# Kernel optimization log

Hardware: AMD Instinct MI355X
Metric: run time of the kernel (lower is better)

The kernel has to match this reference:

```python
import jax, jax.numpy as jnp
import numpy as np
from jax import lax

SIGMA = 2.0
RADIUS = 8  # int(truncate(4.0)*sigma + 0.5) per scipy gaussian_filter

_x = np.arange(-RADIUS, RADIUS + 1, dtype=np.float32)
_gw = np.exp(-0.5 * (_x / SIGMA) ** 2)
GAUSS_W = jnp.asarray(_gw / _gw.sum(), dtype=jnp.float32)  # 17 taps, sums to 1
DERIV_W = jnp.asarray([-1.0, 0.0, 1.0], dtype=jnp.float32)   # scipy correlate1d [-1,0,1]
SMOOTH_W = jnp.asarray([1.0, 2.0, 1.0], dtype=jnp.float32)

DN = ('NCHW', 'OIHW', 'NCHW')

def _corr_h(img, w, pad_mode):
    # 1D cross-correlation along H axis of [B,1,H,W]
    r = w.shape[0] // 2
    p = jnp.pad(img, ((0, 0), (0, 0), (r, r), (0, 0)), mode=pad_mode)
    k = w.reshape(1, 1, -1, 1)
    return lax.conv_general_dilated(p, k, (1, 1), 'VALID', dimension_numbers=DN)

def _corr_w(img, w, pad_mode):
    # 1D cross-correlation along W axis of [B,1,H,W]
    r = w.shape[0] // 2
    p = jnp.pad(img, ((0, 0), (0, 0), (0, 0), (r, r)), mode=pad_mode)
    k = w.reshape(1, 1, 1, -1)
    return lax.conv_general_dilated(p, k, (1, 1), 'VALID', dimension_numbers=DN)

def setup_inputs() -> dict:
    key = jax.random.key(0)
    x = jax.random.normal(key, (32, 3, 512, 512), dtype=jnp.float32)
    return {"x": x}

def reference(x) -> jnp.ndarray:
    # channel mean -> [B,1,H,W]
    g = jnp.mean(x, axis=1, keepdims=True)
    # gaussian blur, scipy mode='reflect' == numpy/jnp 'symmetric' padding
    blur = _corr_w(_corr_h(g, GAUSS_W, 'symmetric'), GAUSS_W, 'symmetric')
    # scipy sobel, mode='constant' (zero pad): deriv along given axis, [1,2,1] smooth along other
    sx = _corr_w(_corr_h(blur, DERIV_W, 'constant'), SMOOTH_W, 'constant')  # axis=0 (H)
    sy = _corr_h(_corr_w(blur, DERIV_W, 'constant'), SMOOTH_W, 'constant')  # axis=1 (W)
    return jnp.hypot(sx, sy)  # [B,1,H,W]
```

## Files before the change

kernel.cpp:

```cpp
#include <hip/hip_runtime.h>
#include <math.h>

#define IMG   512
#define TILE  64
#define HALO  9
#define BROWS 66
#define BSTR  83
#define CSTR  67

__device__ __forceinline__ int reflect_idx(int i) {
    if (i < 0) i = -i - 1;
    if (i >= IMG) i = 2 * IMG - 1 - i;
    return i;
}

__global__ __launch_bounds__(256) void sobel_fused(
    const float* __restrict__ x, float* __restrict__ out)
{
    __shared__ float sB[BROWS * BSTR];
    __shared__ float sC[BROWS * CSTR];

    const int t  = threadIdx.x;
    const int w0 = blockIdx.x * TILE;
    const int h0 = blockIdx.y * TILE;
    const int b  = blockIdx.z;

    const float ge[9] = {1.0f, 0.882496903f, 0.606530660f, 0.324652467f,
                         0.135335283f, 0.0439369336f, 0.0111089965f,
                         0.00218749112f, 0.000335462628f};
    float gw[17];
    {
        float s = 0.f;
        #pragma unroll
        for (int i = 0; i < 17; ++i) { gw[i] = ge[(i < 8) ? (8 - i) : (i - 8)]; s += gw[i]; }
        float inv = 1.0f / s;
        #pragma unroll
        for (int i = 0; i < 17; ++i) gw[i] *= inv;
    }

    const float* xb = x + (size_t)b * 3 * IMG * IMG;
    const float third = 1.0f / 3.0f;

    if (t < 246) {
        int c   = t % 82;
        int seg = t / 82;
        int r0  = seg * 22;
        int gc  = reflect_idx(w0 - HALO + c);
        const float* p0 = xb + gc;
        float v[38];
        #pragma unroll
        for (int i = 0; i < 38; ++i) {
            int gr = reflect_idx(h0 - HALO + r0 + i);
            const float* p = p0 + (size_t)gr * IMG;
            v[i] = (p[0] + p[IMG * IMG] + p[2 * IMG * IMG]) * third;
        }
        #pragma unroll
        for (int j = 0; j < 22; ++j) {
            float a = 0.f;
            #pragma unroll
            for (int k = 0; k < 17; ++k) a += gw[k] * v[j + k];
            sB[(r0 + j) * BSTR + c] = a;
        }
    }
    __syncthreads();

    if (t < 198) {
        int r   = t % 66;
        int seg = t / 66;
        int c0  = seg * 22;
        float v[38];
        #pragma unroll
        for (int i = 0; i < 38; ++i) v[i] = sB[r * BSTR + c0 + i];
        int gr = h0 - 1 + r;
        bool rin = (gr >= 0) & (gr < IMG);
        #pragma unroll
        for (int j = 0; j < 22; ++j) {
            float a = 0.f;
            #pragma unroll
            for (int k = 0; k < 17; ++k) a += gw[k] * v[j + k];
            int gc = w0 - 1 + c0 + j;
            bool in = rin & (gc >= 0) & (gc < IMG);
            sC[r * CSTR + c0 + j] = in ? a : 0.f;
        }
    }
    __syncthreads();

    {
        int c  = t & 63;
        int rq = t >> 6;
        #pragma unroll
        for (int it = 0; it < 4; ++it) {
            int r0 = (rq + it * 4) * 4;
            const float* bp = sC + r0 * CSTR + c;
            float m[6][3];
            #pragma unroll
            for (int rr = 0; rr < 6; ++rr) {
                #pragma unroll
                for (int cc = 0; cc < 3; ++cc)
                    m[rr][cc] = bp[rr * CSTR + cc];
            }
            #pragma unroll
            for (int dr = 0; dr < 4; ++dr) {
                float tl = m[dr][0],   tm = m[dr][1],   tr = m[dr][2];
                float ml = m[dr+1][0],                  mr = m[dr+1][2];
                float bl = m[dr+2][0], bm = m[dr+2][1], br2 = m[dr+2][2];
                float sx = (bl - tl) + 2.f * (bm - tm) + (br2 - tr);
                float sy = (tr - tl) + 2.f * (mr - ml) + (br2 - bl);
                out[((size_t)b * IMG + (h0 + r0 + dr)) * IMG + (w0 + c)]
                    = sqrtf(sx * sx + sy * sy);
            }
        }
    }
}

extern "C" void kernel_launch(void* const* d_in, const int* in_sizes, int n_in,
                              void* d_out, int out_size, void* d_ws, size_t ws_size,
                              hipStream_t stream) {
    const float* x = (const float*)d_in[0];
    float* out = (float*)d_out;
    dim3 grid(IMG / TILE, IMG / TILE, 32);
    dim3 block(256);
    hipLaunchKernelGGL(sobel_fused, grid, block, 0, stream, x, out);
}
```

Before: 167.6 us.

## Blur along W first with float4 row loads, then H from shared memory

Swaps the separable Gaussian pass order so the first pass runs along rows. Each thread loads a contiguous row segment with float4 vector loads over the three channels, which replaces the scalar strided column loads of the old H-first pass. A scalar reflect fallback handles tiles at the image edges. The shared-memory layout changes to match, and launch bounds now request 4 blocks per SM, which may force register spills given the 40-element per-thread arrays.

```diff
diff --git a/kernel.cpp b/kernel.cpp
--- a/kernel.cpp
+++ b/kernel.cpp
@@ -5,8 +5,8 @@
 #define TILE  64
 #define HALO  9
 #define BROWS 66
-#define BSTR  83
-#define CSTR  67
+#define MROWS 82
+#define SSTR  67
 
 __device__ __forceinline__ int reflect_idx(int i) {
     if (i < 0) i = -i - 1;
@@ -14,11 +14,11 @@
     return i;
 }
 
-__global__ __launch_bounds__(256) void sobel_fused(
+__global__ __launch_bounds__(256, 4) void sobel_fused(
     const float* __restrict__ x, float* __restrict__ out)
 {
-    __shared__ float sB[BROWS * BSTR];
-    __shared__ float sC[BROWS * CSTR];
+    __shared__ float sB[MROWS * SSTR];
+    __shared__ float sC[BROWS * SSTR];
 
     const int t  = threadIdx.x;
     const int w0 = blockIdx.x * TILE;
@@ -42,45 +42,68 @@
     const float third = 1.0f / 3.0f;
 
     if (t < 246) {
-        int c   = t % 82;
+        int r   = t % 82;
         int seg = t / 82;
+        int c0  = seg * 24;
+        int gr  = reflect_idx(h0 - HALO + r);
+        const float* rowp = xb + (size_t)gr * IMG;
+        int startc = w0 + c0 - HALO;
+        int abase  = startc - 3;
+        float v[40];
+        if (abase >= 0 && abase + 44 <= IMG) {
+            const float* pa = rowp + abase;
+            #pragma unroll
+            for (int q = 0; q < 11; ++q) {
+                float4 a = *(const float4*)(pa + 4 * q);
+                float4 bb = *(const float4*)(pa + IMG * IMG + 4 * q);
+                float4 cc = *(const float4*)(pa + 2 * IMG * IMG + 4 * q);
+                float m0 = (a.x + bb.x + cc.x) * third;
+                float m1 = (a.y + bb.y + cc.y) * third;
+                float m2 = (a.z + bb.z + cc.z) * third;
+                float m3 = (a.w + bb.w + cc.w) * third;
+                int i0 = 4 * q - 3;
+                if (i0 >= 0)      v[i0]     = m0;
+                if (i0 + 1 >= 0)  v[i0 + 1] = m1;
+                if (i0 + 2 >= 0)  v[i0 + 2] = m2;
+                if (i0 + 3 < 40)  v[i0 + 3] = m3;
+            }
+        } else {
+            #pragma unroll
+            for (int i = 0; i < 40; ++i) {
+                int gc = reflect_idx(startc + i);
+                const float* p = rowp + gc;
+                v[i] = (p[0] + p[IMG * IMG] + p[2 * IMG * IMG]) * third;
+            }
+        }
+        #pragma unroll
+        for (int j = 0; j < 24; ++j) {
+            if (c0 + j < BROWS) {
+                float a = 0.f;
+                #pragma unroll
+                for (int k = 0; k < 17; ++k) a += gw[k] * v[j + k];
+                sB[r * SSTR + c0 + j] = a;
+            }
+        }
+    }
+    __syncthreads();
+
+    if (t < 198) {
+        int c   = t % 66;
+        int seg = t / 66;
         int r0  = seg * 22;
-        int gc  = reflect_idx(w0 - HALO + c);
-        const float* p0 = xb + gc;
         float v[38];
         #pragma unroll
-        for (int i = 0; i < 38; ++i) {
-            int gr = reflect_idx(h0 - HALO + r0 + i);
-            const float* p = p0 + (size_t)gr * IMG;
-            v[i] = (p[0] + p[IMG * IMG] + p[2 * IMG * IMG]) * third;
-        }
+        for (int i = 0; i < 38; ++i) v[i] = sB[(r0 + i) * SSTR + c];
+        int gcol = w0 - 1 + c;
+        bool cin = (gcol >= 0) & (gcol < IMG);
         #pragma unroll
         for (int j = 0; j < 22; ++j) {
             float a = 0.f;
             #pragma unroll
             for (int k = 0; k < 17; ++k) a += gw[k] * v[j + k];
-            sB[(r0 + j) * BSTR + c] = a;
-        }
-    }
-    __syncthreads();
-
-    if (t < 198) {
-        int r   = t % 66;
-        int seg = t / 66;
-        int c0  = seg * 22;
-        float v[38];
-        #pragma unroll
-        for (int i = 0; i < 38; ++i) v[i] = sB[r * BSTR + c0 + i];
-        int gr = h0 - 1 + r;
-        bool rin = (gr >= 0) & (gr < IMG);
-        #pragma unroll
-        for (int j = 0; j < 22; ++j) {
-            float a = 0.f;
-            #pragma unroll
-            for (int k = 0; k < 17; ++k) a += gw[k] * v[j + k];
-            int gc = w0 - 1 + c0 + j;
-            bool in = rin & (gc >= 0) & (gc < IMG);
-            sC[r * CSTR + c0 + j] = in ? a : 0.f;
+            int grow = h0 - 1 + r0 + j;
+            bool in = cin & (grow >= 0) & (grow < IMG);
+            sC[(r0 + j) * SSTR + c] = in ? a : 0.f;
         }
     }
     __syncthreads();
@@ -91,13 +114,13 @@
         #pragma unroll
         for (int it = 0; it < 4; ++it) {
             int r0 = (rq + it * 4) * 4;
-            const float* bp = sC + r0 * CSTR + c;
+            const float* bp = sC + r0 * SSTR + c;
             float m[6][3];
             #pragma unroll
             for (int rr = 0; rr < 6; ++rr) {
                 #pragma unroll
                 for (int cc = 0; cc < 3; ++cc)
-                    m[rr][cc] = bp[rr * CSTR + cc];
+                    m[rr][cc] = bp[rr * SSTR + cc];
             }
             #pragma unroll
             for (int dr = 0; dr < 4; ++dr) {
```

New measurement: 221.7 us. 1.32x slower.

## Shrink tile height to 32 rows and defer channel-mean scaling to output

Applied to the files above, without the earlier changes.

Switches the tile from 64x64 to 64 wide by 32 tall, which doubles the block count and halves shared-memory use per block so more blocks can be resident. Per-thread register arrays shrink in both blur passes and the Sobel stage now computes 8 consecutive rows per thread from one 10x3 window. The divide-by-3 for the channel mean is moved to a single multiply on the final magnitude, which is valid because the blur and Sobel steps are linear. The trade-off is a larger halo share: each 32-row tile re-reads and re-blurs 18 extra rows, so global reads and vertical-blur work per output pixel go up.

```diff
diff --git a/kernel.cpp b/kernel.cpp
--- a/kernel.cpp
+++ b/kernel.cpp
@@ -2,9 +2,10 @@
 #include <math.h>
 
 #define IMG   512
-#define TILE  64
+#define TW    64
+#define TH    32
 #define HALO  9
-#define BROWS 66
+#define HROWS 34
 #define BSTR  83
 #define CSTR  67
 
@@ -17,12 +18,12 @@
 __global__ __launch_bounds__(256) void sobel_fused(
     const float* __restrict__ x, float* __restrict__ out)
 {
-    __shared__ float sB[BROWS * BSTR];
-    __shared__ float sC[BROWS * CSTR];
+    __shared__ float sB[HROWS * BSTR];
+    __shared__ float sC[HROWS * CSTR];
 
     const int t  = threadIdx.x;
-    const int w0 = blockIdx.x * TILE;
-    const int h0 = blockIdx.y * TILE;
+    const int w0 = blockIdx.x * TW;
+    const int h0 = blockIdx.y * TH;
     const int b  = blockIdx.z;
 
     const float ge[9] = {1.0f, 0.882496903f, 0.606530660f, 0.324652467f,
@@ -37,50 +38,52 @@
         #pragma unroll
         for (int i = 0; i < 17; ++i) gw[i] *= inv;
     }
+    const float third = 1.0f / 3.0f;
 
     const float* xb = x + (size_t)b * 3 * IMG * IMG;
-    const float third = 1.0f / 3.0f;
 
     if (t < 246) {
         int c   = t % 82;
         int seg = t / 82;
-        int r0  = seg * 22;
+        int j0  = seg * 12;
         int gc  = reflect_idx(w0 - HALO + c);
-        const float* p0 = xb + gc;
-        float v[38];
+        const float* colp = xb + gc;
+        float v[28];
         #pragma unroll
-        for (int i = 0; i < 38; ++i) {
-            int gr = reflect_idx(h0 - HALO + r0 + i);
-            const float* p = p0 + (size_t)gr * IMG;
-            v[i] = (p[0] + p[IMG * IMG] + p[2 * IMG * IMG]) * third;
+        for (int i = 0; i < 28; ++i) {
+            int gr = reflect_idx(h0 - HALO + j0 + i);
+            const float* p = colp + (size_t)gr * IMG;
+            v[i] = p[0] + p[IMG * IMG] + p[2 * IMG * IMG];
         }
         #pragma unroll
-        for (int j = 0; j < 22; ++j) {
-            float a = 0.f;
-            #pragma unroll
-            for (int k = 0; k < 17; ++k) a += gw[k] * v[j + k];
-            sB[(r0 + j) * BSTR + c] = a;
+        for (int j = 0; j < 12; ++j) {
+            if (j0 + j < HROWS) {
+                float a = 0.f;
+                #pragma unroll
+                for (int k = 0; k < 17; ++k) a += gw[k] * v[j + k];
+                sB[(j0 + j) * BSTR + c] = a;
+            }
         }
     }
     __syncthreads();
 
-    if (t < 198) {
-        int r   = t % 66;
-        int seg = t / 66;
-        int c0  = seg * 22;
-        float v[38];
+    if (t < 204) {
+        int rr  = t % 34;
+        int seg = t / 34;
+        int c0  = seg * 11;
+        float v[27];
         #pragma unroll
-        for (int i = 0; i < 38; ++i) v[i] = sB[r * BSTR + c0 + i];
-        int gr = h0 - 1 + r;
-        bool rin = (gr >= 0) & (gr < IMG);
+        for (int i = 0; i < 27; ++i) v[i] = sB[rr * BSTR + c0 + i];
+        int grow = h0 - 1 + rr;
+        bool rin = (grow >= 0) & (grow < IMG);
         #pragma unroll
-        for (int j = 0; j < 22; ++j) {
+        for (int j = 0; j < 11; ++j) {
             float a = 0.f;
             #pragma unroll
             for (int k = 0; k < 17; ++k) a += gw[k] * v[j + k];
-            int gc = w0 - 1 + c0 + j;
-            bool in = rin & (gc >= 0) & (gc < IMG);
-            sC[r * CSTR + c0 + j] = in ? a : 0.f;
+            int gcol = w0 - 1 + c0 + j;
+            bool in = rin & (gcol >= 0) & (gcol < IMG);
+            sC[rr * CSTR + c0 + j] = in ? a : 0.f;
         }
     }
     __syncthreads();
@@ -88,27 +91,23 @@
     {
         int c  = t & 63;
         int rq = t >> 6;
+        int r0 = rq * 8;
+        float w[10][3];
         #pragma unroll
-        for (int it = 0; it < 4; ++it) {
-            int r0 = (rq + it * 4) * 4;
-            const float* bp = sC + r0 * CSTR + c;
-            float m[6][3];
+        for (int i = 0; i < 10; ++i) {
             #pragma unroll
-            for (int rr = 0; rr < 6; ++rr) {
-                #pragma unroll
-                for (int cc = 0; cc < 3; ++cc)
-                    m[rr][cc] = bp[rr * CSTR + cc];
-            }
-            #pragma unroll
-            for (int dr = 0; dr < 4; ++dr) {
-                float tl = m[dr][0],   tm = m[dr][1],   tr = m[dr][2];
-                float ml = m[dr+1][0],                  mr = m[dr+1][2];
-                float bl = m[dr+2][0], bm = m[dr+2][1], br2 = m[dr+2][2];
-                float sx = (bl - tl) + 2.f * (bm - tm) + (br2 - tr);
-                float sy = (tr - tl) + 2.f * (mr - ml) + (br2 - bl);
-                out[((size_t)b * IMG + (h0 + r0 + dr)) * IMG + (w0 + c)]
-                    = sqrtf(sx * sx + sy * sy);
-            }
+            for (int dc = 0; dc < 3; ++dc)
+                w[i][dc] = sC[(r0 + i) * CSTR + c + dc];
+        }
+        #pragma unroll
+        for (int k = 0; k < 8; ++k) {
+            float tl = w[k][0],     tm = w[k][1],     tr = w[k][2];
+            float ml = w[k + 1][0],                   mr = w[k + 1][2];
+            float bl = w[k + 2][0], bm = w[k + 2][1], br2 = w[k + 2][2];
+            float sx = (bl - tl) + 2.f * (bm - tm) + (br2 - tr);
+            float sy = (tr - tl) + 2.f * (mr - ml) + (br2 - bl);
+            out[((size_t)b * IMG + (h0 + r0 + k)) * IMG + (w0 + c)]
+                = third * sqrtf(sx * sx + sy * sy);
         }
     }
 }
@@ -118,7 +117,7 @@
                               hipStream_t stream) {
     const float* x = (const float*)d_in[0];
     float* out = (float*)d_out;
-    dim3 grid(IMG / TILE, IMG / TILE, 32);
+    dim3 grid(IMG / TW, IMG / TH, 32);
     dim3 block(256);
     hipLaunchKernelGGL(sobel_fused, grid, block, 0, stream, x, out);
 }
```

New measurement: 170.0 us. Within noise of the previous version (+1.4%).
